# Kernel tuning notes

Measured on AMD Instinct MI355X. Metric: run time of the kernel, lower is better.

Reference implementation:

```python
import jax, jax.numpy as jnp
import numpy as np

D_MODEL = 256
NHEAD = 8
HEAD_DIM = D_MODEL // NHEAD
LN_EPS = 1e-5
NEG_INF = -1e30  # finite large-negative; avoids NaN rows while matching masked softmax


def setup_inputs() -> dict:
    key = jax.random.key(0)
    ks = jax.random.split(key, 9)
    B, Q, HW, D = 8, 100, 16384, D_MODEL
    s = 0.02
    return {
        "query": jax.random.normal(ks[0], (B, Q, D), jnp.float32),
        "key_value": jax.random.normal(ks[1], (B, HW, D), jnp.float32),
        "attn_mask": jax.random.randint(ks[2], (B * NHEAD, Q, HW), 0, 2) == 1,  # True = attend
        "in_proj_weight": jax.random.normal(ks[3], (3 * D, D), jnp.float32) * s,
        "in_proj_bias": jax.random.normal(ks[4], (3 * D,), jnp.float32) * s,
        "out_proj_weight": jax.random.normal(ks[5], (D, D), jnp.float32) * s,
        "out_proj_bias": jax.random.normal(ks[6], (D,), jnp.float32) * s,
        "ln_weight": jnp.ones((D,), jnp.float32),
        "ln_bias": jnp.zeros((D,), jnp.float32),
    }


def _mha_masked(query, key_value, attn_mask, in_proj_weight, in_proj_bias,
                out_proj_weight, out_proj_bias):
    B, Q, D = query.shape
    HW = key_value.shape[1]
    Wq, Wk, Wv = jnp.split(in_proj_weight, 3, axis=0)
    bq, bk, bv = jnp.split(in_proj_bias, 3, axis=0)
    q = (query @ Wq.T + bq).reshape(B, Q, NHEAD, HEAD_DIM)
    k = (key_value @ Wk.T + bk).reshape(B, HW, NHEAD, HEAD_DIM)
    v = (key_value @ Wv.T + bv).reshape(B, HW, NHEAD, HEAD_DIM)
    scale = 1.0 / np.sqrt(HEAD_DIM).astype(np.float32)
    scores = jnp.einsum("bqhd,bkhd->bhqk", q, k) * scale  # (B, H, Q, HW)
    attend = attn_mask.reshape(B, NHEAD, Q, HW)  # True = attend
    scores = jnp.where(attend, scores, NEG_INF)
    probs = jax.nn.softmax(scores, axis=-1)
    ctx = jnp.einsum("bhqk,bkhd->bqhd", probs, v).reshape(B, Q, D)
    return ctx @ out_proj_weight.T + out_proj_bias


def reference(query, key_value, attn_mask, in_proj_weight, in_proj_bias,
              out_proj_weight, out_proj_bias, ln_weight, ln_bias):
    attn_out = _mha_masked(query, key_value, attn_mask, in_proj_weight,
                           in_proj_bias, out_proj_weight, out_proj_bias)
    x = query + attn_out  # dropout p=0.0 is identity
    mu = jnp.mean(x, axis=-1, keepdims=True)
    var = jnp.mean(jnp.square(x - mu), axis=-1, keepdims=True)
    return (x - mu) * jax.lax.rsqrt(var + LN_EPS) * ln_weight + ln_bias
```

## Files before the change

kernel.cpp:

```cpp
#include <hip/hip_runtime.h>
#include <stdint.h>

#define BB   8
#define NH   8
#define QQ   100
#define HWK  16384
#define DM   256
#define HD   32
#define QP   112
#define MT   7
#define NPART 64
#define SCALE2 0.2550602534365564f

typedef short bf16x8 __attribute__((ext_vector_type(8)));
typedef float f32x4  __attribute__((ext_vector_type(4)));
typedef unsigned int u32x4 __attribute__((ext_vector_type(4)));
typedef unsigned short u16;
typedef unsigned int   u32;
typedef unsigned long long u64;

__device__ __forceinline__ u16 f2bf(float f) {
  u32 u = __builtin_bit_cast(u32, f);
  u += 0x7fffu + ((u >> 16) & 1u);
  return (u16)(u >> 16);
}
__device__ __forceinline__ u16 f2bf_ru(float f) {
  return (u16)((__builtin_bit_cast(u32, f) + 0x8000u) >> 16);
}
__device__ __forceinline__ u32 pack2rn(float lo, float hi) {
  u32 a = __builtin_bit_cast(u32, lo) + 0x8000u;
  u32 b = __builtin_bit_cast(u32, hi) + 0x8000u;
  return __builtin_amdgcn_perm(b, a, 0x07060302u);
}
__device__ __forceinline__ float bf_lo(u32 u) {
  return __builtin_bit_cast(float, u << 16);
}
__device__ __forceinline__ float bf_hi(u32 u) {
  return __builtin_bit_cast(float, u & 0xffff0000u);
}
__device__ __forceinline__ float fast_exp2(float x) {
#if __has_builtin(__builtin_amdgcn_exp2f)
  return __builtin_amdgcn_exp2f(x);
#else
  return exp2f(x);
#endif
}

__global__ __launch_bounds__(256) void wconv_kernel(
    const float* __restrict__ W, u16* __restrict__ wbf) {
  const int i = (blockIdx.x * 256 + threadIdx.x) * 4;
  const float4 w = *(const float4*)(W + 256 * DM + i);
  u32* dst = (u32*)(wbf + i);
  dst[0] = pack2rn(w.x, w.y);
  dst[1] = pack2rn(w.z, w.w);
}

__global__ __launch_bounds__(256) void proj_q_kernel(
    const float* __restrict__ query, const float* __restrict__ W,
    const float* __restrict__ bias, u16* __restrict__ q_bf) {
  __shared__ float xrow[DM];
  const int bq = blockIdx.x;
  const int b = bq / QQ, qi = bq % QQ;
  const int tid = threadIdx.x;
  if (tid < 64)
    ((float4*)xrow)[tid] = ((const float4*)(query + (size_t)bq * DM))[tid];
  __syncthreads();
  const int j = tid;
  float acc = bias[j];
  const float4* wr = (const float4*)(W + (size_t)j * DM);
  #pragma unroll 8
  for (int c = 0; c < 64; ++c) {
    float4 w = wr[c];
    float4 x = ((const float4*)xrow)[c];
    acc += w.x * x.x + w.y * x.y + w.z * x.z + w.w * x.w;
  }
  acc *= SCALE2;
  const int h = j >> 5, d = j & 31;
  q_bf[(((size_t)(b * NH + h)) * QQ + qi) * HD + d] = f2bf(acc);
}

__global__ __launch_bounds__(256) void proj_kv_kernel(
    const float* __restrict__ kv, const u16* __restrict__ wbf,
    const float* __restrict__ bias, u16* __restrict__ k_bf,
    u16* __restrict__ v_t) {
  __shared__ u16 Tl[4][5120];
  const int rb = blockIdx.x;
  const size_t m0 = (size_t)rb * 64;
  const int tid = threadIdx.x, lane = tid & 63, wid = tid >> 6;
  const int lane15 = lane & 15, quad = lane >> 4;
  const int jw = wid * 128;

  f32x4 acc[4][8];
  #pragma unroll
  for (int mi = 0; mi < 4; ++mi)
    #pragma unroll
    for (int ni = 0; ni < 8; ++ni) acc[mi][ni] = (f32x4){0.f, 0.f, 0.f, 0.f};

  for (int ks = 0; ks < 8; ++ks) {
    bf16x8 afr[4];
    #pragma unroll
    for (int mi = 0; mi < 4; ++mi) {
      const float* ap = kv + (m0 + mi * 16 + lane15) * DM + ks * 32 + quad * 8;
      float4 a0 = ((const float4*)ap)[0];
      float4 a1 = ((const float4*)ap)[1];
      uint4 w;
      w.x = pack2rn(a0.x, a0.y); w.y = pack2rn(a0.z, a0.w);
      w.z = pack2rn(a1.x, a1.y); w.w = pack2rn(a1.z, a1.w);
      afr[mi] = __builtin_bit_cast(bf16x8, w);
    }
    #pragma unroll
    for (int ni = 0; ni < 8; ++ni) {
      bf16x8 bfr = __builtin_bit_cast(bf16x8,
          *(const uint4*)(wbf + (size_t)(jw + ni * 16 + lane15) * DM + ks * 32 + quad * 8));
      #pragma unroll
      for (int mi = 0; mi < 4; ++mi)
        acc[mi][ni] = __builtin_amdgcn_mfma_f32_16x16x32_bf16(afr[mi], bfr, acc[mi][ni], 0, 0, 0);
    }
  }

  u16* T = Tl[wid];
  const float* bptr = bias + 256 + jw;
  if (wid < 2) {
    #pragma unroll
    for (int p = 0; p < 2; ++p) {
      #pragma unroll
      for (int mm = 0; mm < 2; ++mm) {
        const int mi = p * 2 + mm;
        #pragma unroll
        for (int ni = 0; ni < 8; ++ni) {
          const float bv = bptr[ni * 16 + lane15];
          #pragma unroll
          for (int r = 0; r < 4; ++r)
            T[(mm * 16 + quad * 4 + r) * 136 + ni * 16 + lane15] =
                f2bf_ru(acc[mi][ni][r] + bv);
        }
      }
      #pragma unroll
      for (int it = 0; it < 8; ++it) {
        const int row = it * 4 + quad;
        const int c0 = lane15 * 8;
        uint4 val = *(const uint4*)&T[row * 136 + c0];
        const size_t m = m0 + p * 32 + row;
        const size_t b = m >> 14, key = m & 16383;
        const int col256 = jw + c0;
        const int h = col256 >> 5, d = col256 & 31;
        *(uint4*)&k_bf[((b * NH + h) * HWK + key) * HD + d] = val;
      }
    }
  } else {
    const int jwv = jw - 256;
    #pragma unroll
    for (int p = 0; p < 2; ++p) {
      #pragma unroll
      for (int mm = 0; mm < 2; ++mm) {
        const int mi = p * 2 + mm;
        #pragma unroll
        for (int ni = 0; ni < 8; ++ni) {
          const float bv = bptr[ni * 16 + lane15];
          u32* dst = (u32*)&T[(ni * 16 + lane15) * 40 + mm * 16 + quad * 4];
          dst[0] = pack2rn(acc[mi][ni][0] + bv, acc[mi][ni][1] + bv);
          dst[1] = pack2rn(acc[mi][ni][2] + bv, acc[mi][ni][3] + bv);
        }
      }
      #pragma unroll
      for (int it = 0; it < 8; ++it) {
        const int col = it * 16 + (lane >> 2);
        const int koff = (lane & 3) * 8;
        uint4 val = *(const uint4*)&T[col * 40 + koff];
        const size_t m = m0 + p * 32 + koff;
        const size_t b = m >> 14, key = m & 16383;
        const int col256 = jwv + col;
        const int h = col256 >> 5, d = col256 & 31;
        *(uint4*)&v_t[((b * NH + h) * HD + d) * HWK + key] = val;
      }
    }
  }
}

__global__ __launch_bounds__(256) void attn_kernel(
    const u16* __restrict__ q_bf, const u16* __restrict__ k_bf,
    const u16* __restrict__ v_t, const int* __restrict__ mask,
    float* __restrict__ l_p, u32* __restrict__ ctxp) {
  __shared__ u16 qlds[QP * 40];
  __shared__ u32 mb[QP * 52];
  const int tid = threadIdx.x;
  const int lane = tid & 63, wid = tid >> 6;
  const int lane15 = lane & 15, quad = lane >> 4;
  const int bh = blockIdx.x >> 4, chunk = blockIdx.x & 15;

  for (int i = tid; i < QP * HD; i += 256) {
    const int row = i >> 5, d = i & 31;
    qlds[row * 40 + d] = (row < QQ) ? q_bf[((size_t)bh * QQ + row) * HD + d] : (u16)0;
  }
  for (int i = tid; i < 12 * 52; i += 256) mb[QQ * 52 + i] = 0u;

  {
    const int* mp_base = mask + (size_t)bh * QQ * HWK + chunk * 1024;
    for (int rr = 0; rr < 25; ++rr) {
      const int row = wid * 25 + rr;
      const int* mp = mp_base + (size_t)row * HWK;
      int4 v[4];
      #pragma unroll
      for (int q = 0; q < 4; ++q) v[q] = ((const int4*)(mp + q * 256))[lane];
      #pragma unroll
      for (int q = 0; q < 4; ++q) {
        const u64 b0 = __ballot(v[q].x != 0);
        const u64 b1 = __ballot(v[q].y != 0);
        const u64 b2 = __ballot(v[q].z != 0);
        const u64 b3 = __ballot(v[q].w != 0);
        if (lane < 8) {
          const int j = lane >> 1;
          const u64 bj = (j == 0) ? b0 : (j == 1) ? b1 : (j == 2) ? b2 : b3;
          mb[row * 52 + q * 12 + (lane & 1) * 4 + j] =
              (lane & 1) ? (u32)(bj >> 32) : (u32)bj;
        }
      }
    }
  }
  __syncthreads();

  const int klocal_base = wid * 256;
  const int key_base = chunk * 1024 + klocal_base;
  const u16* kbase = k_bf + (size_t)bh * HWK * HD;
  const u16* vtb  = v_t  + (size_t)bh * HWK * HD;

  const int sl_lo = lane15 + 32 * (quad & 1);
  const int sl_hi = sl_lo + 16;
  const u32 selperm = (quad & 2) ? 0x07060302u : 0x05040100u;

  f32x4 acc[MT][2];
  float l_run[MT];
  #pragma unroll
  for (int mt = 0; mt < MT; ++mt) {
    acc[mt][0] = (f32x4){0.f, 0.f, 0.f, 0.f};
    acc[mt][1] = (f32x4){0.f, 0.f, 0.f, 0.f};
    l_run[mt] = 0.f;
  }

  for (int kg = 0; kg < 8; ++kg) {
    const int key0 = key_base + kg * 32;
    const int mwoff = wid * 12 + ((kg & 4) ? 4 : 0);
    const int sh = ((kg & 3) << 3) + quad;
    bf16x8 kf0 = __builtin_bit_cast(bf16x8,
        *(const uint4*)(kbase + (size_t)(key0 + lane15) * HD + quad * 8));
    bf16x8 kf1 = __builtin_bit_cast(bf16x8,
        *(const uint4*)(kbase + (size_t)(key0 + 16 + lane15) * HD + quad * 8));
    bf16x8 vf0 = __builtin_bit_cast(bf16x8,
        *(const uint4*)(vtb + (size_t)lane15 * HWK + key0 + quad * 8));
    bf16x8 vf1 = __builtin_bit_cast(bf16x8,
        *(const uint4*)(vtb + (size_t)(lane15 + 16) * HWK + key0 + quad * 8));
    #pragma unroll
    for (int mt = 0; mt < MT; ++mt) {
      const int rowg = mt * 16 + lane15;
      bf16x8 af = __builtin_bit_cast(bf16x8,
          *(const uint4*)&qlds[rowg * 40 + quad * 8]);
      u32x4 mw = *(const u32x4*)&mb[rowg * 52 + mwoff];
      const f32x4 zero = {0.f, 0.f, 0.f, 0.f};
      f32x4 s0 = __builtin_amdgcn_mfma_f32_16x16x32_bf16(kf0, af, zero, 0, 0, 0);
      f32x4 s1 = __builtin_amdgcn_mfma_f32_16x16x32_bf16(kf1, af, zero, 0, 0, 0);
      u32 pk[4];
      float lsum = 0.f;
      #pragma unroll
      for (int r = 0; r < 4; ++r) {
        const float p0 = ((mw[r] >> sh) & 1u)       ? fast_exp2(s0[r]) : 0.f;
        const float p1 = ((mw[r] >> (sh + 4)) & 1u) ? fast_exp2(s1[r]) : 0.f;
        lsum += p0 + p1;
        pk[r] = pack2rn(p0, p1);
      }
      l_run[mt] += lsum;
      u32 wA0 = (u32)__shfl((int)pk[0], sl_lo);
      u32 wA1 = (u32)__shfl((int)pk[1], sl_lo);
      u32 wA2 = (u32)__shfl((int)pk[2], sl_lo);
      u32 wA3 = (u32)__shfl((int)pk[3], sl_lo);
      u32 wB0 = (u32)__shfl((int)pk[0], sl_hi);
      u32 wB1 = (u32)__shfl((int)pk[1], sl_hi);
      u32 wB2 = (u32)__shfl((int)pk[2], sl_hi);
      u32 wB3 = (u32)__shfl((int)pk[3], sl_hi);
      uint4 pw;
      pw.x = __builtin_amdgcn_perm(wA1, wA0, selperm);
      pw.y = __builtin_amdgcn_perm(wA3, wA2, selperm);
      pw.z = __builtin_amdgcn_perm(wB1, wB0, selperm);
      pw.w = __builtin_amdgcn_perm(wB3, wB2, selperm);
      bf16x8 pf = __builtin_bit_cast(bf16x8, pw);
      acc[mt][0] = __builtin_amdgcn_mfma_f32_16x16x32_bf16(vf0, pf, acc[mt][0], 0, 0, 0);
      acc[mt][1] = __builtin_amdgcn_mfma_f32_16x16x32_bf16(vf1, pf, acc[mt][1], 0, 0, 0);
    }
  }

  const int part = chunk * 4 + wid;
  #pragma unroll
  for (int mt = 0; mt < MT; ++mt) {
    const int row = mt * 16 + lane15;
    float lr = l_run[mt];
    lr += __shfl_xor(lr, 16);
    lr += __shfl_xor(lr, 32);
    const size_t base = ((size_t)bh * QP + row) * NPART + part;
    if (quad == 0) l_p[base] = lr;
    uint2 lo2, hi2;
    lo2.x = pack2rn(acc[mt][0][0], acc[mt][0][1]);
    lo2.y = pack2rn(acc[mt][0][2], acc[mt][0][3]);
    hi2.x = pack2rn(acc[mt][1][0], acc[mt][1][1]);
    hi2.y = pack2rn(acc[mt][1][2], acc[mt][1][3]);
    *(uint2*)&ctxp[base * 16 + quad * 2]     = lo2;
    *(uint2*)&ctxp[base * 16 + 8 + quad * 2] = hi2;
  }
}

__global__ __launch_bounds__(256) void combine_kernel(
    const float* __restrict__ l_p, const u32* __restrict__ ctxp,
    const float* __restrict__ query, const float* __restrict__ Wo,
    const float* __restrict__ bo, const float* __restrict__ lnw,
    const float* __restrict__ lnb, float* __restrict__ out) {
  __shared__ float ctx_row[DM];
  __shared__ float red[8];
  const int bq = blockIdx.x;
  const int b = bq / QQ, qi = bq % QQ;
  const int tid = threadIdx.x, lane = tid & 63, wid = tid >> 6;

  for (int hh = 0; hh < 2; ++hh) {
    const int h = wid * 2 + hh;
    const size_t base = ((size_t)(b * NH + h) * QP + qi) * NPART;
    float lv = l_p[base + lane];
    #pragma unroll
    for (int o = 1; o < 64; o <<= 1) lv += __shfl_xor(lv, o);
    const float inv_l = 1.0f / lv;
    const int c = lane & 7, pg = lane >> 3;
    const u32* cp = ctxp + base * 16 + c * 2;
    float s0 = 0.f, s1 = 0.f, s2 = 0.f, s3 = 0.f;
    for (int p = pg; p < NPART; p += 8) {
      uint2 u = *(const uint2*)(cp + (size_t)p * 16);
      s0 += bf_lo(u.x); s1 += bf_hi(u.x);
      s2 += bf_lo(u.y); s3 += bf_hi(u.y);
    }
    #pragma unroll
    for (int o = 8; o < 64; o <<= 1) {
      s0 += __shfl_xor(s0, o);
      s1 += __shfl_xor(s1, o);
      s2 += __shfl_xor(s2, o);
      s3 += __shfl_xor(s3, o);
    }
    if (pg == 0) {
      ctx_row[h * HD + c * 4]     = s0 * inv_l;
      ctx_row[h * HD + c * 4 + 1] = s1 * inv_l;
      ctx_row[h * HD + c * 4 + 2] = s2 * inv_l;
      ctx_row[h * HD + c * 4 + 3] = s3 * inv_l;
    }
  }
  __syncthreads();

  const int j = tid;
  float s = bo[j];
  const float4* wr = (const float4*)(Wo + (size_t)j * DM);
  #pragma unroll 8
  for (int c = 0; c < 64; ++c) {
    float4 wv = wr[c];
    float4 cx = ((const float4*)ctx_row)[c];
    s += wv.x * cx.x + wv.y * cx.y + wv.z * cx.z + wv.w * cx.w;
  }
  const float x = s + query[(size_t)bq * DM + j];

  float t = x;
  #pragma unroll
  for (int o = 1; o < 64; o <<= 1) t += __shfl_xor(t, o);
  if (lane == 0) red[wid] = t;
  __syncthreads();
  const float mu = (red[0] + red[1] + red[2] + red[3]) * (1.0f / DM);
  const float dx = x - mu;
  float t2 = dx * dx;
  #pragma unroll
  for (int o = 1; o < 64; o <<= 1) t2 += __shfl_xor(t2, o);
  if (lane == 0) red[4 + wid] = t2;
  __syncthreads();
  const float var = (red[4] + red[5] + red[6] + red[7]) * (1.0f / DM);
  out[(size_t)bq * DM + j] = dx * rsqrtf(var + 1e-5f) * lnw[j] + lnb[j];
}

extern "C" void kernel_launch(void* const* d_in, const int* in_sizes, int n_in,
                              void* d_out, int out_size, void* d_ws, size_t ws_size,
                              hipStream_t stream) {
  const float* query = (const float*)d_in[0];
  const float* kv    = (const float*)d_in[1];
  const int*   mask  = (const int*)d_in[2];
  const float* ipw   = (const float*)d_in[3];
  const float* ipb   = (const float*)d_in[4];
  const float* opw   = (const float*)d_in[5];
  const float* opb   = (const float*)d_in[6];
  const float* lnw   = (const float*)d_in[7];
  const float* lnb   = (const float*)d_in[8];
  float* out = (float*)d_out;

  char* ws = (char*)d_ws;
  u16*   k_bf  = (u16*)(ws);
  u16*   v_t   = (u16*)(ws + 67108864);
  u16*   q_bf  = (u16*)(ws + 134217728);
  float* l_p   = (float*)(ws + 134742016);
  u32*   ctxp  = (u32*)(ws + 136577024);
  u16*   wbf   = (u16*)(ws + 195297280);

  wconv_kernel  <<<128,          256, 0, stream>>>(ipw, wbf);
  proj_q_kernel <<<BB * QQ,      256, 0, stream>>>(query, ipw, ipb, q_bf);
  proj_kv_kernel<<<2048,         256, 0, stream>>>(kv, wbf, ipb, k_bf, v_t);
  attn_kernel   <<<BB * NH * 16, 256, 0, stream>>>(q_bf, k_bf, v_t, mask, l_p, ctxp);
  combine_kernel<<<BB * QQ,      256, 0, stream>>>(l_p, ctxp, query, opw, opb, lnw, lnb, out);
}
```

Before: 870.1 us.

## Move mask bit-packing into KV projection kernel and merge weight conversion with Q projection

The mask-to-bitmask compaction moves out of the attention kernel into extra blocks of the KV projection launch, interleaved one in three, and the packed bits go to a global workspace. This lets the memory-bound mask read overlap with the compute-bound projection. The weight conversion kernel is folded into the Q projection launch, saving one launch. The attention kernel drops its LDS staging of Q and the mask and reads both straight from global memory, which costs an extra global read of the packed mask per block.

```diff
diff --git a/kernel.cpp b/kernel.cpp
--- a/kernel.cpp
+++ b/kernel.cpp
@@ -14,7 +14,6 @@
 
 typedef short bf16x8 __attribute__((ext_vector_type(8)));
 typedef float f32x4  __attribute__((ext_vector_type(4)));
-typedef unsigned int u32x4 __attribute__((ext_vector_type(4)));
 typedef unsigned short u16;
 typedef unsigned int   u32;
 typedef unsigned long long u64;
@@ -46,22 +45,23 @@
 #endif
 }
 
-__global__ __launch_bounds__(256) void wconv_kernel(
-    const float* __restrict__ W, u16* __restrict__ wbf) {
-  const int i = (blockIdx.x * 256 + threadIdx.x) * 4;
-  const float4 w = *(const float4*)(W + 256 * DM + i);
-  u32* dst = (u32*)(wbf + i);
-  dst[0] = pack2rn(w.x, w.y);
-  dst[1] = pack2rn(w.z, w.w);
-}
-
-__global__ __launch_bounds__(256) void proj_q_kernel(
+__global__ __launch_bounds__(256) void qw_kernel(
     const float* __restrict__ query, const float* __restrict__ W,
-    const float* __restrict__ bias, u16* __restrict__ q_bf) {
+    const float* __restrict__ bias, u16* __restrict__ q_bf,
+    u16* __restrict__ wbf) {
   __shared__ float xrow[DM];
-  const int bq = blockIdx.x;
+  const int bid = blockIdx.x;
+  const int tid = threadIdx.x;
+  if (bid >= BB * QQ) {
+    const int i = ((bid - BB * QQ) * 256 + tid) * 4;
+    const float4 w = *(const float4*)(W + 256 * DM + i);
+    u32* dst = (u32*)(wbf + i);
+    dst[0] = pack2rn(w.x, w.y);
+    dst[1] = pack2rn(w.z, w.w);
+    return;
+  }
+  const int bq = bid;
   const int b = bq / QQ, qi = bq % QQ;
-  const int tid = threadIdx.x;
   if (tid < 64)
     ((float4*)xrow)[tid] = ((const float4*)(query + (size_t)bq * DM))[tid];
   __syncthreads();
@@ -79,14 +79,44 @@
   q_bf[(((size_t)(b * NH + h)) * QQ + qi) * HD + d] = f2bf(acc);
 }
 
-__global__ __launch_bounds__(256) void proj_kv_kernel(
+__global__ __launch_bounds__(256) void kvcp_kernel(
     const float* __restrict__ kv, const u16* __restrict__ wbf,
-    const float* __restrict__ bias, u16* __restrict__ k_bf,
-    u16* __restrict__ v_t) {
+    const float* __restrict__ bias, const int* __restrict__ mask,
+    u16* __restrict__ k_bf, u16* __restrict__ v_t, u32* __restrict__ mbg) {
   __shared__ u16 Tl[4][5120];
-  const int rb = blockIdx.x;
+  const int bid = blockIdx.x;
+  const int tid = threadIdx.x, lane = tid & 63, wid = tid >> 6;
+
+  if (bid % 3 == 2) {
+    const int cpid = bid / 3;
+    const int bh = cpid >> 4, chunk = cpid & 15;
+    const int* mp_base = mask + (size_t)bh * QQ * HWK + chunk * 1024;
+    u32* dst_base = mbg + (size_t)cpid * QP * 32;
+    for (int rr = 0; rr < 25; ++rr) {
+      const int row = wid * 25 + rr;
+      const int* mp = mp_base + (size_t)row * HWK;
+      int4 v[4];
+      #pragma unroll
+      for (int q = 0; q < 4; ++q) v[q] = ((const int4*)(mp + q * 256))[lane];
+      #pragma unroll
+      for (int q = 0; q < 4; ++q) {
+        const u64 b0 = __ballot(v[q].x != 0);
+        const u64 b1 = __ballot(v[q].y != 0);
+        const u64 b2 = __ballot(v[q].z != 0);
+        const u64 b3 = __ballot(v[q].w != 0);
+        if (lane < 8) {
+          const int j = lane >> 1;
+          const u64 bj = (j == 0) ? b0 : (j == 1) ? b1 : (j == 2) ? b2 : b3;
+          dst_base[row * 32 + q * 8 + (lane & 1) * 4 + j] =
+              (lane & 1) ? (u32)(bj >> 32) : (u32)bj;
+        }
+      }
+    }
+    return;
+  }
+
+  const int rb = (bid / 3) * 2 + (bid % 3);
   const size_t m0 = (size_t)rb * 64;
-  const int tid = threadIdx.x, lane = tid & 63, wid = tid >> 6;
   const int lane15 = lane & 15, quad = lane >> 4;
   const int jw = wid * 128;
 
@@ -179,50 +209,18 @@
 
 __global__ __launch_bounds__(256) void attn_kernel(
     const u16* __restrict__ q_bf, const u16* __restrict__ k_bf,
-    const u16* __restrict__ v_t, const int* __restrict__ mask,
+    const u16* __restrict__ v_t, const u32* __restrict__ mbg,
     float* __restrict__ l_p, u32* __restrict__ ctxp) {
-  __shared__ u16 qlds[QP * 40];
-  __shared__ u32 mb[QP * 52];
   const int tid = threadIdx.x;
   const int lane = tid & 63, wid = tid >> 6;
   const int lane15 = lane & 15, quad = lane >> 4;
   const int bh = blockIdx.x >> 4, chunk = blockIdx.x & 15;
 
-  for (int i = tid; i < QP * HD; i += 256) {
-    const int row = i >> 5, d = i & 31;
-    qlds[row * 40 + d] = (row < QQ) ? q_bf[((size_t)bh * QQ + row) * HD + d] : (u16)0;
-  }
-  for (int i = tid; i < 12 * 52; i += 256) mb[QQ * 52 + i] = 0u;
-
-  {
-    const int* mp_base = mask + (size_t)bh * QQ * HWK + chunk * 1024;
-    for (int rr = 0; rr < 25; ++rr) {
-      const int row = wid * 25 + rr;
-      const int* mp = mp_base + (size_t)row * HWK;
-      int4 v[4];
-      #pragma unroll
-      for (int q = 0; q < 4; ++q) v[q] = ((const int4*)(mp + q * 256))[lane];
-      #pragma unroll
-      for (int q = 0; q < 4; ++q) {
-        const u64 b0 = __ballot(v[q].x != 0);
-        const u64 b1 = __ballot(v[q].y != 0);
-        const u64 b2 = __ballot(v[q].z != 0);
-        const u64 b3 = __ballot(v[q].w != 0);
-        if (lane < 8) {
-          const int j = lane >> 1;
-          const u64 bj = (j == 0) ? b0 : (j == 1) ? b1 : (j == 2) ? b2 : b3;
-          mb[row * 52 + q * 12 + (lane & 1) * 4 + j] =
-              (lane & 1) ? (u32)(bj >> 32) : (u32)bj;
-        }
-      }
-    }
-  }
-  __syncthreads();
-
-  const int klocal_base = wid * 256;
-  const int key_base = chunk * 1024 + klocal_base;
+  const int key_base = chunk * 1024 + wid * 256;
   const u16* kbase = k_bf + (size_t)bh * HWK * HD;
   const u16* vtb  = v_t  + (size_t)bh * HWK * HD;
+  const u16* qb   = q_bf + (size_t)bh * QQ * HD;
+  const u32* mrow = mbg + (size_t)blockIdx.x * QP * 32 + wid * 8;
 
   const int sl_lo = lane15 + 32 * (quad & 1);
   const int sl_hi = sl_lo + 16;
@@ -239,7 +237,7 @@
 
   for (int kg = 0; kg < 8; ++kg) {
     const int key0 = key_base + kg * 32;
-    const int mwoff = wid * 12 + ((kg & 4) ? 4 : 0);
+    const int h4 = (kg & 4) ? 4 : 0;
     const int sh = ((kg & 3) << 3) + quad;
     bf16x8 kf0 = __builtin_bit_cast(bf16x8,
         *(const uint4*)(kbase + (size_t)(key0 + lane15) * HD + quad * 8));
@@ -253,11 +251,13 @@
     for (int mt = 0; mt < MT; ++mt) {
       const int rowg = mt * 16 + lane15;
       bf16x8 af = __builtin_bit_cast(bf16x8,
-          *(const uint4*)&qlds[rowg * 40 + quad * 8]);
-      u32x4 mw = *(const u32x4*)&mb[rowg * 52 + mwoff];
+          *(const uint4*)(qb + (size_t)rowg * HD + quad * 8));
+      uint4 mwv = *(const uint4*)(mrow + rowg * 32 + h4);
+      if (mt == MT - 1 && rowg >= QQ) mwv = (uint4){0u, 0u, 0u, 0u};
       const f32x4 zero = {0.f, 0.f, 0.f, 0.f};
       f32x4 s0 = __builtin_amdgcn_mfma_f32_16x16x32_bf16(kf0, af, zero, 0, 0, 0);
       f32x4 s1 = __builtin_amdgcn_mfma_f32_16x16x32_bf16(kf1, af, zero, 0, 0, 0);
+      const u32 mw[4] = {mwv.x, mwv.y, mwv.z, mwv.w};
       u32 pk[4];
       float lsum = 0.f;
       #pragma unroll
@@ -396,10 +396,10 @@
   float* l_p   = (float*)(ws + 134742016);
   u32*   ctxp  = (u32*)(ws + 136577024);
   u16*   wbf   = (u16*)(ws + 195297280);
-
-  wconv_kernel  <<<128,          256, 0, stream>>>(ipw, wbf);
-  proj_q_kernel <<<BB * QQ,      256, 0, stream>>>(query, ipw, ipb, q_bf);
-  proj_kv_kernel<<<2048,         256, 0, stream>>>(kv, wbf, ipb, k_bf, v_t);
-  attn_kernel   <<<BB * NH * 16, 256, 0, stream>>>(q_bf, k_bf, v_t, mask, l_p, ctxp);
-  combine_kernel<<<BB * QQ,      256, 0, stream>>>(l_p, ctxp, query, opw, opb, lnw, lnb, out);
-}
+  u32*   mbg   = (u32*)(ws + 195559424);
+
+  qw_kernel     <<<BB * QQ + 128, 256, 0, stream>>>(query, ipw, ipb, q_bf, wbf);
+  kvcp_kernel   <<<3072,          256, 0, stream>>>(kv, wbf, ipb, mask, k_bf, v_t, mbg);
+  attn_kernel   <<<BB * NH * 16,  256, 0, stream>>>(q_bf, k_bf, v_t, mbg, l_p, ctxp);
+  combine_kernel<<<BB * QQ,       256, 0, stream>>>(l_p, ctxp, query, opw, opb, lnw, lnb, out);
+}
```

Measured after the change: 908.0 us. 4.3% more time.
